# Performance work log

Hardware: AMD Instinct MI355X
Metric: run time of the kernel (lower is better)

Reference implementation:

```python
import jax, jax.numpy as jnp
import numpy as np

B, S, D, P, NQ = 8, 2048, 1024, 256, 8192


def setup_inputs() -> dict:
    key = jax.random.key(0)
    ks = jax.random.split(key, 8)
    return {
        "flag": 0,
        "encoded_input": jax.random.normal(ks[0], (B, S, D), dtype=jnp.float32),
        "start_ids_1": jax.random.randint(ks[1], (NQ,), 0, S, dtype=jnp.int32),
        "end_ids_1": jax.random.randint(ks[2], (NQ,), 0, S, dtype=jnp.int32),
        "query_batch_idx": jax.random.randint(ks[3], (NQ,), 0, B, dtype=jnp.int32),
        "start_ids_2": jax.random.randint(ks[4], (NQ,), 0, S, dtype=jnp.int32),
        "end_ids_2": jax.random.randint(ks[5], (NQ,), 0, S, dtype=jnp.int32),
        "W": jax.random.normal(ks[6], (D, P), dtype=jnp.float32) * 0.02,
        "b": jnp.zeros((P,), dtype=jnp.float32),
    }


def _gather_spans(h, qb, s, e):
    # span_repr[b, i, j] = concat(h[b, i], h[b, j]) for j >= i, else 0.
    # Direct gather instead of building the O(seq^2) table.
    rep = jnp.concatenate([h[qb, s], h[qb, e]], axis=-1)  # [NQ, 2*P]
    valid = (e >= s).astype(rep.dtype)[:, None]
    return rep * valid


def reference(flag, encoded_input, start_ids_1, end_ids_1, query_batch_idx,
              start_ids_2, end_ids_2, W, b):
    h = encoded_input @ W + b  # [B, S, P] (use_proj=True)
    res1 = _gather_spans(h, query_batch_idx, start_ids_1, end_ids_1)
    res2 = _gather_spans(h, query_batch_idx, start_ids_2, end_ids_2)
    return (res1, res2)
```

## Files before the change

### kernel.cpp

```cpp
#include <hip/hip_runtime.h>
#include <hip/hip_bf16.h>
#include <stdint.h>

#define S_LEN 2048
#define D_DIM 1024
#define P_DIM 256
#define NQ_   8192
#define M_TOT 16384

#define BM 64
#define BN 256
#define BK 64
#define CAP 32
#define HS  260

typedef __attribute__((ext_vector_type(4))) float  f32x4;
typedef __attribute__((ext_vector_type(8))) __bf16 bf16x8;

__device__ __forceinline__ void async16(const void* g, void* l) {
    __builtin_amdgcn_global_load_lds(
        (const __attribute__((address_space(1))) uint32_t*)g,
        (__attribute__((address_space(3))) uint32_t*)l, 16, 0, 0);
}

__global__ __launch_bounds__(1024) void wt_kernel(const float* __restrict__ W,
                                                  __bf16* __restrict__ WT,
                                                  int* __restrict__ cnt) {
    __shared__ __bf16 tile[32][33];
    const int k0 = blockIdx.x * 32;
    const int n0 = blockIdx.y * 32;
    const int tx = threadIdx.x, ty = threadIdx.y;
    const int g = (blockIdx.y * gridDim.x + blockIdx.x) * 1024 + ty * 32 + tx;
    if (g < M_TOT) cnt[g] = 0;
    tile[ty][tx] = (__bf16)W[(k0 + ty) * P_DIM + (n0 + tx)];
    __syncthreads();
    WT[(n0 + ty) * D_DIM + (k0 + tx)] = tile[tx][ty];
}

__global__ __launch_bounds__(256) void index_zero(const int* __restrict__ s1,
                                                  const int* __restrict__ e1,
                                                  const int* __restrict__ s2,
                                                  const int* __restrict__ e2,
                                                  const int* __restrict__ qb,
                                                  int* __restrict__ cnt,
                                                  int* __restrict__ bucket,
                                                  float* __restrict__ out) {
    const int q    = blockIdx.x * 256 + threadIdx.x;
    const int lane = threadIdx.x & 63;
    const int bqw  = blockIdx.x * 256 + (threadIdx.x & ~63);
    const int b    = qb[q];
    const float4 z = make_float4(0.f, 0.f, 0.f, 0.f);
    #pragma unroll
    for (int set = 0; set < 2; ++set) {
        const int s = set ? s2[q] : s1[q];
        const int e = set ? e2[q] : e1[q];
        if (e >= s) {
            int r = b * S_LEN + s;
            int k = atomicAdd(&cnt[r], 1); if (k < CAP) bucket[r * CAP + k] = (q << 2) | (set << 1);
            r = b * S_LEN + e;
            k = atomicAdd(&cnt[r], 1);     if (k < CAP) bucket[r * CAP + k] = (q << 2) | (set << 1) | 1;
        }
        unsigned long long mask = __ballot(e < s);
        while (mask) {
            const int j = __ffsll(mask) - 1;
            mask &= mask - 1;
            const int qz = bqw + j;
            float4* dst = (float4*)(out + (size_t)set * (NQ_ * 512) + (size_t)qz * 512);
            dst[lane]      = z;
            dst[lane + 64] = z;
        }
    }
}

__global__ __launch_bounds__(256, 1) void gemm_kernel(const float*  __restrict__ A,
                                                      const __bf16* __restrict__ WT,
                                                      const float*  __restrict__ bias,
                                                      const int*    __restrict__ cnt,
                                                      const int*    __restrict__ bucket,
                                                      float*        __restrict__ out) {
    __shared__ __align__(16) char smem[2 * BM * BK * 2 + 2 * BN * BK * 2];
    __shared__ int s_cnt[64];
    __shared__ int s_off[65];
    __shared__ int elist[64 * CAP];

    const int tid = threadIdx.x;
    const int w   = tid >> 6;
    const int l   = tid & 63;
    const int lm  = l & 15;
    const int q   = l >> 4;

    const int m0 = blockIdx.x * BM;

    auto bufA = [&](int buf) -> __bf16* { return (__bf16*)smem + buf * (BM * BK); };
    auto bufB = [&](int buf) -> __bf16* { return (__bf16*)(smem + 2 * BM * BK * 2) + buf * (BN * BK); };

    const int brow_l = l >> 3;
    const int bc     = (l & 7) ^ (brow_l & 7);

    auto stageB = [&](int buf, int k0) {
        __bf16* B = bufB(buf);
        #pragma unroll
        for (int j = 0; j < 8; ++j) {
            const int r   = w * 8 + j;
            const int row = r * 8 + brow_l;
            const __bf16* g = WT + (size_t)row * D_DIM + k0 + bc * 8;
            async16(g, B + r * 512);
        }
    };

    const int arow = tid >> 2;
    const int ac   = tid & 3;
    const float* agp = A + (size_t)(m0 + arow) * D_DIM + ac * 16;
    const int p0 = ((2 * ac)     ^ (arow & 7)) * 8;
    const int p1 = ((2 * ac + 1) ^ (arow & 7)) * 8;

    float4 fa[4];
    auto loadA = [&](int k0) {
        #pragma unroll
        for (int i = 0; i < 4; ++i) fa[i] = *(const float4*)(agp + k0 + 4 * i);
    };
    auto writeA = [&](int buf) {
        bf16x8 v0, v1;
        v0[0] = (__bf16)fa[0].x; v0[1] = (__bf16)fa[0].y; v0[2] = (__bf16)fa[0].z; v0[3] = (__bf16)fa[0].w;
        v0[4] = (__bf16)fa[1].x; v0[5] = (__bf16)fa[1].y; v0[6] = (__bf16)fa[1].z; v0[7] = (__bf16)fa[1].w;
        v1[0] = (__bf16)fa[2].x; v1[1] = (__bf16)fa[2].y; v1[2] = (__bf16)fa[2].z; v1[3] = (__bf16)fa[2].w;
        v1[4] = (__bf16)fa[3].x; v1[5] = (__bf16)fa[3].y; v1[6] = (__bf16)fa[3].z; v1[7] = (__bf16)fa[3].w;
        __bf16* Ab = bufA(buf) + arow * BK;
        *(bf16x8*)(Ab + p0) = v0;
        *(bf16x8*)(Ab + p1) = v1;
    };

    f32x4 acc[4][4] = {};

    auto compute = [&](int buf) {
        const __bf16* Ab = bufA(buf);
        const __bf16* Bb = bufB(buf);
        #pragma unroll
        for (int kh = 0; kh < 2; ++kh) {
            const int pos = ((kh * 4 + q) ^ (lm & 7)) * 8;
            bf16x8 af[4], bfr[4];
            #pragma unroll
            for (int mi = 0; mi < 4; ++mi)
                af[mi] = *(const bf16x8*)(Ab + (mi * 16 + lm) * BK + pos);
            #pragma unroll
            for (int ni = 0; ni < 4; ++ni)
                bfr[ni] = *(const bf16x8*)(Bb + (w * 64 + ni * 16 + lm) * BK + pos);
            #pragma unroll
            for (int mi = 0; mi < 4; ++mi)
                #pragma unroll
                for (int ni = 0; ni < 4; ++ni)
                    acc[mi][ni] = __builtin_amdgcn_mfma_f32_16x16x32_bf16(
                        af[mi], bfr[ni], acc[mi][ni], 0, 0, 0);
        }
    };

    loadA(0);
    stageB(0, 0);
    writeA(0);
    __syncthreads();

    #pragma unroll 1
    for (int p = 0; p < 7; ++p) {
        const int k1 = (2 * p + 1) * BK, k2 = (2 * p + 2) * BK;
        loadA(k1); stageB(1, k1);
        __builtin_amdgcn_sched_barrier(0);
        compute(0);
        __builtin_amdgcn_sched_barrier(0);
        writeA(1);
        __syncthreads();
        loadA(k2); stageB(0, k2);
        __builtin_amdgcn_sched_barrier(0);
        compute(1);
        __builtin_amdgcn_sched_barrier(0);
        writeA(0);
        __syncthreads();
    }
    {
        const int k1 = 15 * BK;
        loadA(k1); stageB(1, k1);
        __builtin_amdgcn_sched_barrier(0);
        compute(0);
        __builtin_amdgcn_sched_barrier(0);
        writeA(1);
        __syncthreads();
    }
    compute(1);

    __syncthreads();
    float* hs = (float*)smem;

    if (tid < 64) { int c = cnt[m0 + tid]; s_cnt[tid] = c < CAP ? c : CAP; }

    #pragma unroll
    for (int ni = 0; ni < 4; ++ni) {
        const int col = w * 64 + ni * 16 + lm;
        const float bv = bias[col];
        #pragma unroll
        for (int mi = 0; mi < 4; ++mi) {
            const int rbase = mi * 16 + q * 4;
            #pragma unroll
            for (int r = 0; r < 4; ++r)
                hs[(rbase + r) * HS + col] = acc[mi][ni][r] + bv;
        }
    }
    __syncthreads();
    if (tid == 0) {
        int a = 0;
        #pragma unroll 1
        for (int i = 0; i < 64; ++i) { s_off[i] = a; a += s_cnt[i]; }
        s_off[64] = a;
    }
    __syncthreads();
    if (tid < 64) {
        const int o = s_off[tid], c = s_cnt[tid];
        const int* bk = bucket + (size_t)(m0 + tid) * CAP;
        for (int k = 0; k < c; ++k)
            elist[o + k] = (tid << 15) | (bk[k] & 0x7fff);
    }
    __syncthreads();

    const int E   = s_off[64];
    const int grp = tid >> 6;
    const int gl  = tid & 63;
    #pragma unroll 1
    for (int j = grp; j < E; j += 4) {
        const int ent  = elist[j];
        const int rl   = ent >> 15;
        const int code = ent & 0x7fff;
        const int qq   = code >> 2;
        const int st   = (code >> 1) & 1;
        const int hf   = code & 1;
        const float4 v = *(const float4*)&hs[rl * HS + gl * 4];
        *(float4*)(out + (size_t)st * (NQ_ * 512) + (size_t)qq * 512 + hf * 256 + gl * 4) = v;
    }
}

extern "C" void kernel_launch(void* const* d_in, const int* in_sizes, int n_in,
                              void* d_out, int out_size, void* d_ws, size_t ws_size,
                              hipStream_t stream) {
    const float* A    = (const float*)d_in[1];
    const int*   s1   = (const int*)  d_in[2];
    const int*   e1   = (const int*)  d_in[3];
    const int*   qb   = (const int*)  d_in[4];
    const int*   s2   = (const int*)  d_in[5];
    const int*   e2   = (const int*)  d_in[6];
    const float* W    = (const float*)d_in[7];
    const float* bias = (const float*)d_in[8];
    float*       out  = (float*)d_out;

    __bf16* WT     = (__bf16*)d_ws;
    int*    cnt    = (int*)((char*)d_ws + (1 << 20));
    int*    bucket = (int*)((char*)d_ws + (1 << 20) + (1 << 16));

    wt_kernel  <<<dim3(32, 8), dim3(32, 32), 0, stream>>>(W, WT, cnt);
    index_zero <<<dim3(NQ_ / 256), dim3(256), 0, stream>>>(s1, e1, s2, e2, qb, cnt, bucket, out);
    gemm_kernel<<<dim3(M_TOT / BM), dim3(256), 0, stream>>>(A, WT, bias, cnt, bucket, out);
}
```

Baseline: 147.9 us.

## Triple-buffer B tiles with manual vmcnt waits for deeper prefetch

Adds a third LDS buffer for the weight tile so B loads are issued two K-steps ahead, and replaces __syncthreads with raw s_barrier plus explicit vmcnt/lgkmcnt waits. The aim is to hide global-to-LDS latency behind MFMA compute and drop the full memory drain each iteration. In exchange it uses more LDS, and correctness now depends on hand-counted outstanding-load numbers that must match the exact instructions issued by stageB and loadA.

```diff
diff --git a/kernel.cpp b/kernel.cpp
--- a/kernel.cpp
+++ b/kernel.cpp
@@ -78,7 +78,7 @@
                                                       const int*    __restrict__ cnt,
                                                       const int*    __restrict__ bucket,
                                                       float*        __restrict__ out) {
-    __shared__ __align__(16) char smem[2 * BM * BK * 2 + 2 * BN * BK * 2];
+    __shared__ __align__(16) char smem[2 * BM * BK * 2 + 3 * BN * BK * 2];
     __shared__ int s_cnt[64];
     __shared__ int s_off[65];
     __shared__ int elist[64 * CAP];
@@ -132,9 +132,9 @@
 
     f32x4 acc[4][4] = {};
 
-    auto compute = [&](int buf) {
-        const __bf16* Ab = bufA(buf);
-        const __bf16* Bb = bufB(buf);
+    auto compute = [&](int bufa, int bufb) {
+        const __bf16* Ab = bufA(bufa);
+        const __bf16* Bb = bufB(bufb);
         #pragma unroll
         for (int kh = 0; kh < 2; ++kh) {
             const int pos = ((kh * 4 + q) ^ (lm & 7)) * 8;
@@ -156,35 +156,29 @@
 
     loadA(0);
     stageB(0, 0);
+    stageB(1, BK);
     writeA(0);
-    __syncthreads();
+    loadA(BK);
+    asm volatile("s_waitcnt lgkmcnt(0)");
+    __builtin_amdgcn_sched_barrier(0);
 
     #pragma unroll 1
-    for (int p = 0; p < 7; ++p) {
-        const int k1 = (2 * p + 1) * BK, k2 = (2 * p + 2) * BK;
-        loadA(k1); stageB(1, k1);
-        __builtin_amdgcn_sched_barrier(0);
-        compute(0);
-        __builtin_amdgcn_sched_barrier(0);
-        writeA(1);
-        __syncthreads();
-        loadA(k2); stageB(0, k2);
-        __builtin_amdgcn_sched_barrier(0);
-        compute(1);
-        __builtin_amdgcn_sched_barrier(0);
-        writeA(0);
-        __syncthreads();
-    }
-    {
-        const int k1 = 15 * BK;
-        loadA(k1); stageB(1, k1);
-        __builtin_amdgcn_sched_barrier(0);
-        compute(0);
-        __builtin_amdgcn_sched_barrier(0);
-        writeA(1);
-        __syncthreads();
-    }
-    compute(1);
+    for (int i = 0; i < 16; ++i) {
+        __builtin_amdgcn_sched_barrier(0);
+        if (i == 0)       asm volatile("s_waitcnt vmcnt(12)");
+        else if (i == 15) asm volatile("s_waitcnt vmcnt(0)");
+        else              asm volatile("s_waitcnt vmcnt(16)");
+        __builtin_amdgcn_s_barrier();
+        __builtin_amdgcn_sched_barrier(0);
+        if (i <= 13) stageB((i + 2) % 3, (i + 2) * BK);
+        __builtin_amdgcn_sched_barrier(0);
+        compute(i & 1, i % 3);
+        __builtin_amdgcn_sched_barrier(0);
+        if (i <= 14) writeA((i + 1) & 1);
+        if (i <= 13) loadA((i + 2) * BK);
+        asm volatile("s_waitcnt lgkmcnt(0)");
+        __builtin_amdgcn_sched_barrier(0);
+    }
 
     __syncthreads();
     float* hs = (float*)smem;
```

Result: no change. 148.9 us (+0.7%).

## Pre-convert A tile to swizzled bf16 scratch and triple-buffer async loads

Applied to the files above, without the earlier changes.

Each block first converts its 64-row fp32 A slice to bf16 in a pre-swizzled layout in workspace memory. The main loop then stages A and B with async global-to-LDS loads through a three-buffer pipeline using vmcnt waits, instead of register-staged A conversion. This aims to overlap memory latency with MFMA compute and remove per-step conversion work from the loop. In exchange it adds a full extra write and read pass over A through global memory (likely served from L2) and uses more LDS.

```diff
diff --git a/kernel.cpp b/kernel.cpp
--- a/kernel.cpp
+++ b/kernel.cpp
@@ -77,8 +77,9 @@
                                                       const float*  __restrict__ bias,
                                                       const int*    __restrict__ cnt,
                                                       const int*    __restrict__ bucket,
+                                                      __bf16*       __restrict__ Abf,
                                                       float*        __restrict__ out) {
-    __shared__ __align__(16) char smem[2 * BM * BK * 2 + 2 * BN * BK * 2];
+    __shared__ __align__(16) char smem[3 * BM * BK * 2 + 3 * BN * BK * 2];
     __shared__ int s_cnt[64];
     __shared__ int s_off[65];
     __shared__ int elist[64 * CAP];
@@ -92,42 +93,52 @@
     const int m0 = blockIdx.x * BM;
 
     auto bufA = [&](int buf) -> __bf16* { return (__bf16*)smem + buf * (BM * BK); };
-    auto bufB = [&](int buf) -> __bf16* { return (__bf16*)(smem + 2 * BM * BK * 2) + buf * (BN * BK); };
+    auto bufB = [&](int buf) -> __bf16* { return (__bf16*)(smem + 3 * BM * BK * 2) + buf * (BN * BK); };
+
+    {
+        const float* src = A   + (size_t)m0 * D_DIM;
+        __bf16*      dst = Abf + (size_t)m0 * D_DIM;
+        #pragma unroll 4
+        for (int it = 0; it < 32; ++it) {
+            const int f  = it * 2048 + tid * 8;
+            const int rr = f >> 10;
+            const int k  = f & 1023;
+            const float4 x0 = *(const float4*)(src + f);
+            const float4 x1 = *(const float4*)(src + f + 4);
+            bf16x8 v;
+            v[0] = (__bf16)x0.x; v[1] = (__bf16)x0.y; v[2] = (__bf16)x0.z; v[3] = (__bf16)x0.w;
+            v[4] = (__bf16)x1.x; v[5] = (__bf16)x1.y; v[6] = (__bf16)x1.z; v[7] = (__bf16)x1.w;
+            const int c   = k >> 3;
+            const int kt  = c >> 3;
+            const int pos = (c & 7) ^ (rr & 7);
+            *(bf16x8*)(dst + kt * 4096 + rr * 64 + pos * 8) = v;
+        }
+    }
+    asm volatile("s_waitcnt vmcnt(0)");
+    __builtin_amdgcn_s_barrier();
+    __builtin_amdgcn_sched_barrier(0);
+
+    const __bf16* Ap = Abf + (size_t)m0 * D_DIM;
+
+    auto stageA = [&](int buf, int s) {
+        __bf16* dA = bufA(buf);
+        #pragma unroll
+        for (int u = 0; u < 2; ++u) {
+            const int jj = w * 2 + u;
+            async16(Ap + s * 4096 + jj * 512 + l * 8, dA + jj * 512);
+        }
+    };
 
     const int brow_l = l >> 3;
     const int bc     = (l & 7) ^ (brow_l & 7);
-
-    auto stageB = [&](int buf, int k0) {
+    auto stageB = [&](int buf, int s) {
         __bf16* B = bufB(buf);
         #pragma unroll
         for (int j = 0; j < 8; ++j) {
             const int r   = w * 8 + j;
             const int row = r * 8 + brow_l;
-            const __bf16* g = WT + (size_t)row * D_DIM + k0 + bc * 8;
-            async16(g, B + r * 512);
-        }
-    };
-
-    const int arow = tid >> 2;
-    const int ac   = tid & 3;
-    const float* agp = A + (size_t)(m0 + arow) * D_DIM + ac * 16;
-    const int p0 = ((2 * ac)     ^ (arow & 7)) * 8;
-    const int p1 = ((2 * ac + 1) ^ (arow & 7)) * 8;
-
-    float4 fa[4];
-    auto loadA = [&](int k0) {
-        #pragma unroll
-        for (int i = 0; i < 4; ++i) fa[i] = *(const float4*)(agp + k0 + 4 * i);
-    };
-    auto writeA = [&](int buf) {
-        bf16x8 v0, v1;
-        v0[0] = (__bf16)fa[0].x; v0[1] = (__bf16)fa[0].y; v0[2] = (__bf16)fa[0].z; v0[3] = (__bf16)fa[0].w;
-        v0[4] = (__bf16)fa[1].x; v0[5] = (__bf16)fa[1].y; v0[6] = (__bf16)fa[1].z; v0[7] = (__bf16)fa[1].w;
-        v1[0] = (__bf16)fa[2].x; v1[1] = (__bf16)fa[2].y; v1[2] = (__bf16)fa[2].z; v1[3] = (__bf16)fa[2].w;
-        v1[4] = (__bf16)fa[3].x; v1[5] = (__bf16)fa[3].y; v1[6] = (__bf16)fa[3].z; v1[7] = (__bf16)fa[3].w;
-        __bf16* Ab = bufA(buf) + arow * BK;
-        *(bf16x8*)(Ab + p0) = v0;
-        *(bf16x8*)(Ab + p1) = v1;
+            async16(WT + (size_t)row * D_DIM + s * BK + bc * 8, B + r * 512);
+        }
     };
 
     f32x4 acc[4][4] = {};
@@ -154,37 +165,35 @@
         }
     };
 
-    loadA(0);
-    stageB(0, 0);
-    writeA(0);
-    __syncthreads();
+    stageA(0, 0); stageB(0, 0);
+    stageA(1, 1); stageB(1, 1);
+
+#define STEP(s, bcur, bnext, dostage)                          \
+    asm volatile("s_waitcnt vmcnt(10)");                       \
+    __builtin_amdgcn_sched_barrier(0);                         \
+    __builtin_amdgcn_s_barrier();                              \
+    __builtin_amdgcn_sched_barrier(0);                         \
+    if (dostage) { stageA(bnext, (s) + 2); stageB(bnext, (s) + 2); } \
+    __builtin_amdgcn_sched_barrier(0);                         \
+    compute(bcur);                                             \
+    __builtin_amdgcn_sched_barrier(0);
 
     #pragma unroll 1
-    for (int p = 0; p < 7; ++p) {
-        const int k1 = (2 * p + 1) * BK, k2 = (2 * p + 2) * BK;
-        loadA(k1); stageB(1, k1);
-        __builtin_amdgcn_sched_barrier(0);
-        compute(0);
-        __builtin_amdgcn_sched_barrier(0);
-        writeA(1);
-        __syncthreads();
-        loadA(k2); stageB(0, k2);
-        __builtin_amdgcn_sched_barrier(0);
-        compute(1);
-        __builtin_amdgcn_sched_barrier(0);
-        writeA(0);
-        __syncthreads();
-    }
-    {
-        const int k1 = 15 * BK;
-        loadA(k1); stageB(1, k1);
-        __builtin_amdgcn_sched_barrier(0);
-        compute(0);
-        __builtin_amdgcn_sched_barrier(0);
-        writeA(1);
-        __syncthreads();
-    }
-    compute(1);
+    for (int j = 0; j < 4; ++j) {
+        const int s0 = j * 3;
+        STEP(s0,     0, 2, 1)
+        STEP(s0 + 1, 1, 0, 1)
+        STEP(s0 + 2, 2, 1, 1)
+    }
+    STEP(12, 0, 2, 1)
+    STEP(13, 1, 0, 1)
+    STEP(14, 2, 1, 0)
+    asm volatile("s_waitcnt vmcnt(0)");
+    __builtin_amdgcn_sched_barrier(0);
+    __builtin_amdgcn_s_barrier();
+    __builtin_amdgcn_sched_barrier(0);
+    compute(0);
+#undef STEP
 
     __syncthreads();
     float* hs = (float*)smem;
@@ -251,8 +260,9 @@
     __bf16* WT     = (__bf16*)d_ws;
     int*    cnt    = (int*)((char*)d_ws + (1 << 20));
     int*    bucket = (int*)((char*)d_ws + (1 << 20) + (1 << 16));
+    __bf16* Abf    = (__bf16*)((char*)d_ws + (16 << 20));
 
     wt_kernel  <<<dim3(32, 8), dim3(32, 32), 0, stream>>>(W, WT, cnt);
     index_zero <<<dim3(NQ_ / 256), dim3(256), 0, stream>>>(s1, e1, s2, e2, qb, cnt, bucket, out);
-    gemm_kernel<<<dim3(M_TOT / BM), dim3(256), 0, stream>>>(A, WT, bias, cnt, bucket, out);
-}
+    gemm_kernel<<<dim3(M_TOT / BM), dim3(256), 0, stream>>>(A, WT, bias, cnt, bucket, Abf, out);
+}
```

Result: slower. 154.7 us (+4.6%).
